# Optimization experiments

Measured on AMD Instinct MI355X. Metric: run time of the kernel, lower is better.

Reference implementation:

```python
import jax, jax.numpy as jnp
import numpy as np

B, HF, WF = 16, 32, 32
DIM, NH = 1024, 16
HD = DIM // NH  # 64


def axial_freqs(H, W, head_dim):
    # RotaryEmbedding(dim=head_dim//4, freqs_for='pixel', max_freq=H*W)
    d = head_dim // 4  # rotary dim per axis
    base = jnp.linspace(1.0, (H * W) / 2.0, d // 2) * jnp.pi  # [d//2]
    posH = jnp.linspace(-1.0, 1.0, H)
    posW = jnp.linspace(-1.0, 1.0, W)
    fH = jnp.repeat(posH[:, None] * base[None, :], 2, axis=-1)  # [H, d]
    fW = jnp.repeat(posW[:, None] * base[None, :], 2, axis=-1)  # [W, d]
    fH = jnp.broadcast_to(fH[:, None, :], (H, W, d))
    fW = jnp.broadcast_to(fW[None, :, :], (H, W, d))
    return jnp.concatenate([fH, fW], axis=-1)  # [H, W, 2d] = [H, W, head_dim//2]


def rotate_half(x):
    # interleaved pair rotation: (x1, x2) -> (-x2, x1)
    xr = x.reshape(*x.shape[:-1], -1, 2)
    x1, x2 = xr[..., 0], xr[..., 1]
    return jnp.stack([-x2, x1], axis=-1).reshape(x.shape)


def apply_rotary(freqs, t):
    # t: [B, h, H, W, hd]; freqs: [H, W, rot_dim]
    rd = freqs.shape[-1]
    t_rot, t_pass = t[..., :rd], t[..., rd:]
    t_rot = t_rot * jnp.cos(freqs) + rotate_half(t_rot) * jnp.sin(freqs)
    return jnp.concatenate([t_rot, t_pass], axis=-1)


def setup_inputs() -> dict:
    key = jax.random.key(0)
    k1, k2, k3 = jax.random.split(key, 3)
    s = 1.0 / np.sqrt(DIM)
    return {
        "x": jax.random.normal(k1, (B, HF * WF, DIM), jnp.float32),
        "w_qkv": jax.random.normal(k2, (3 * DIM, DIM), jnp.float32) * s,
        "w_proj": jax.random.normal(k3, (DIM, DIM), jnp.float32) * s,
        "b_proj": jnp.zeros((DIM,), jnp.float32),
    }


def reference(x, w_qkv, w_proj, b_proj):
    freqs = axial_freqs(HF, WF, HD)
    qkv = x @ w_qkv.T  # [B, N, 3*DIM]
    q, k, v = jnp.split(qkv, 3, axis=-1)

    def to_grid(t):  # [B, N, DIM] -> [B, h, H, W, hd]
        return t.reshape(B, HF, WF, NH, HD).transpose(0, 3, 1, 2, 4)

    q, k, v = to_grid(q), to_grid(k), to_grid(v)
    q = apply_rotary(freqs, q)
    k = apply_rotary(freqs, k)
    N = HF * WF
    q = q.reshape(B, NH, N, HD)
    k = k.reshape(B, NH, N, HD)
    v = v.reshape(B, NH, N, HD)

    scale = 1.0 / np.sqrt(HD)
    attn = jax.nn.softmax(jnp.einsum('bhnd,bhmd->bhnm', q, k) * scale, axis=-1)
    out = jnp.einsum('bhnm,bhmd->bhnd', attn, v)  # [B, h, N, hd]
    out = out.transpose(0, 2, 1, 3).reshape(B, N, DIM)
    return out @ w_proj.T + b_proj
```

## Files before the change

### kernel.cpp

```cpp
#include <hip/hip_runtime.h>
#include <hip/hip_bf16.h>
#include <math.h>

typedef __bf16 bf16;
typedef bf16 bf16x4 __attribute__((ext_vector_type(4)));
typedef bf16 bf16x8 __attribute__((ext_vector_type(8)));
typedef float f32x4 __attribute__((ext_vector_type(4)));

#define MFMA16(a, b, c) __builtin_amdgcn_mfma_f32_16x16x32_bf16((a), (b), (c), 0, 0, 0)

#define QSCALE 0.18033688011112042f

__device__ __forceinline__ void async16(const void* g, void* l) {
  __builtin_amdgcn_global_load_lds(
      (const __attribute__((address_space(1))) void*)g,
      (__attribute__((address_space(3))) void*)l, 16, 0, 0);
}

__global__ __launch_bounds__(256) void f2b_kernel(const float* __restrict__ in,
                                                  bf16* __restrict__ out, int n) {
  int i = (blockIdx.x * 256 + threadIdx.x) * 4;
  if (i >= n) return;
  f32x4 v = *(const f32x4*)(in + i);
  bf16x4 o = {(bf16)v[0], (bf16)v[1], (bf16)v[2], (bf16)v[3]};
  *(bf16x4*)(out + i) = o;
}

__global__ __launch_bounds__(256) void table_kernel(float* __restrict__ cosT,
                                                    float* __restrict__ sinT) {
  int idx = blockIdx.x * 256 + threadIdx.x;
  if (idx >= 1024 * 32) return;
  int n = idx >> 5, d = idx & 31;
  int hf = n >> 5, wf = n & 31;
  int bi = (d & 15) >> 1;
  float base = (1.0f + 73.0f * bi) * 3.14159265358979323846f;
  int p = (d < 16) ? hf : wf;
  float pos = (2.0f * (float)p - 31.0f) * (1.0f / 31.0f);
  float f = pos * base;
  cosT[idx] = cosf(f);
  sinT[idx] = sinf(f);
}

template <int EPI, int NBN>
__global__ __launch_bounds__(512, 2) void gemm_bt(
    const bf16* __restrict__ A, const bf16* __restrict__ W,
    bf16* __restrict__ oq, bf16* __restrict__ okk, bf16* __restrict__ ovt,
    const float* __restrict__ cosT, const float* __restrict__ sinT,
    float* __restrict__ outF, const float* __restrict__ bias) {
  constexpr int K = 1024;
  __shared__ bf16 As[4][256 * 32];
  __shared__ bf16 Bs[4][256 * 32];

  const int tid = threadIdx.x;
  const int lane = tid & 63;
  const int wid = tid >> 6;
  const int lo = lane & 15, hi = lane >> 4;
  const int wm = wid >> 2;
  const int wn = wid & 3;

  const int wg = blockIdx.x;
  const int xcd = wg & 7;
  const int i = wg >> 3;
  const int s = i >> 4;
  const int r = i & 15;
  const int bm = xcd * 8 + (s & 1) * 4 + (r & 3);
  const int bn = (s >> 1) * 4 + (r >> 2);

  const bf16* Ab = A + (size_t)bm * 256 * K;
  const bf16* Wb = W + (size_t)bn * 256 * K;

  const f32x4 fzero = {0.f, 0.f, 0.f, 0.f};
  f32x4 acc[8][4];
#pragma unroll
  for (int i2 = 0; i2 < 8; ++i2)
#pragma unroll
    for (int j = 0; j < 4; ++j) acc[i2][j] = fzero;

  size_t srcOff[2];
  int ldsOff[2];
#pragma unroll
  for (int i2 = 0; i2 < 2; ++i2) {
    const int c = i2 * 512 + tid;
    const int row = c >> 2, g = c & 3;
    const int gsrc = g ^ ((row >> 1) & 3);
    srcOff[i2] = (size_t)row * K + gsrc * 8;
    ldsOff[i2] = c * 8;
  }

  auto stageSlot = [&](int slot, int kh) {
#pragma unroll
    for (int i2 = 0; i2 < 2; ++i2)
      async16(Ab + srcOff[i2] + kh * 32, &As[slot][ldsOff[i2]]);
#pragma unroll
    for (int i2 = 0; i2 < 2; ++i2)
      async16(Wb + srcOff[i2] + kh * 32, &Bs[slot][ldsOff[i2]]);
  };

  auto compute = [&](int slot) {
    bf16x8 af[8], bf[4];
#pragma unroll
    for (int mf = 0; mf < 8; ++mf) {
      const int row = wm * 128 + mf * 16 + lo;
      const int g = hi ^ ((row >> 1) & 3);
      af[mf] = *(const bf16x8*)&As[slot][row * 32 + g * 8];
    }
#pragma unroll
    for (int nf = 0; nf < 4; ++nf) {
      const int row = wn * 64 + nf * 16 + lo;
      const int g = hi ^ ((row >> 1) & 3);
      bf[nf] = *(const bf16x8*)&Bs[slot][row * 32 + g * 8];
    }
    __builtin_amdgcn_s_setprio(1);
#pragma unroll
    for (int mf = 0; mf < 8; ++mf)
#pragma unroll
      for (int nf = 0; nf < 4; ++nf)
        acc[mf][nf] = MFMA16(af[mf], bf[nf], acc[mf][nf]);
    __builtin_amdgcn_s_setprio(0);
  };

  stageSlot(0, 0);
  stageSlot(1, 1);

  for (int kt = 0; kt < 7; ++kt) {
#pragma unroll
    for (int ph = 0; ph < 4; ++ph) {
      stageSlot((ph + 2) & 3, kt * 4 + ph + 2);
      asm volatile("s_waitcnt vmcnt(8)" ::: "memory");
      __builtin_amdgcn_s_barrier();
      compute(ph);
    }
  }
  stageSlot(2, 30);
  asm volatile("s_waitcnt vmcnt(8)" ::: "memory");
  __builtin_amdgcn_s_barrier();
  compute(0);
  stageSlot(3, 31);
  asm volatile("s_waitcnt vmcnt(8)" ::: "memory");
  __builtin_amdgcn_s_barrier();
  compute(1);
  asm volatile("s_waitcnt vmcnt(4)" ::: "memory");
  __builtin_amdgcn_s_barrier();
  compute(2);
  asm volatile("s_waitcnt vmcnt(0)" ::: "memory");
  __builtin_amdgcn_s_barrier();
  compute(3);

  const int rb0 = bm * 256 + wm * 128;
  const int jb0 = bn * 256 + wn * 64;

  if constexpr (EPI == 0) {
#pragma unroll
    for (int ac = 0; ac < 4; ++ac) {
      const int j = jb0 + ac * 16 + lo;
      const int which = j >> 10;
      const int f = j & 1023;
      const int h = f >> 6, d = f & 63;
#pragma unroll
      for (int ar = 0; ar < 8; ++ar) {
        const int rb = rb0 + ar * 16 + 4 * hi;
        f32x4 v = acc[ar][ac];
        if (which == 2) {
          const int b = rb >> 10, n0 = rb & 1023;
          bf16x4 pk = {(bf16)v[0], (bf16)v[1], (bf16)v[2], (bf16)v[3]};
          *(bf16x4*)(ovt + ((size_t)((b * 16 + h) * 64 + d)) * 1024 + n0) = pk;
        } else {
          bf16* dst = which ? okk : oq;
          const float sc = which ? 1.0f : QSCALE;
#pragma unroll
          for (int reg = 0; reg < 4; ++reg) {
            const int r2 = rb + reg;
            const int b = r2 >> 10, n = r2 & 1023;
            float val = v[reg];
            float res;
            if (d < 32) {
              float c = cosT[n * 32 + d];
              float sn = sinT[n * 32 + d];
              float pp = __shfl_xor(val, 1);
              res = (d & 1) ? fmaf(val, c, pp * sn) : fmaf(val, c, -(pp * sn));
            } else {
              res = val;
            }
            dst[((size_t)((b * 16 + h) * 1024 + n)) * 64 + d] = (bf16)(res * sc);
          }
        }
      }
    }
  } else {
#pragma unroll
    for (int ac = 0; ac < 4; ++ac) {
      const int j = jb0 + ac * 16 + lo;
      const float bv = bias[j];
#pragma unroll
      for (int ar = 0; ar < 8; ++ar) {
        const int rb = rb0 + ar * 16 + 4 * hi;
#pragma unroll
        for (int reg = 0; reg < 4; ++reg)
          outF[(size_t)(rb + reg) * 1024 + j] = acc[ar][ac][reg] + bv;
      }
    }
  }
}

__global__ __launch_bounds__(512, 4) void attn_fwd(const bf16* __restrict__ q,
                                                   const bf16* __restrict__ k,
                                                   const bf16* __restrict__ vt,
                                                   bf16* __restrict__ o) {
  __shared__ bf16 Kt[2][64 * 64];
  __shared__ bf16 Vt[2][64 * 64];
  __shared__ bf16 Pt[8][32 * 68];
  const int tid = threadIdx.x;
  const int lane = tid & 63, wid = tid >> 6;
  const int lo = lane & 15, hi = lane >> 4;
  const int j = blockIdx.x;
  const int bh = (j & 7) + ((j >> 5) << 3);
  const int qt = (j >> 3) & 3;
  const bf16* qg = q + (size_t)bh * 65536;
  const bf16* kg = k + (size_t)bh * 65536;
  const bf16* vg = vt + (size_t)bh * 65536;

  bf16x8 qf[2][2];
#pragma unroll
  for (int rg = 0; rg < 2; ++rg) {
    const int qrow = qt * 256 + wid * 32 + rg * 16 + lo;
#pragma unroll
    for (int ch = 0; ch < 2; ++ch)
      qf[rg][ch] = *(const bf16x8*)(qg + (size_t)qrow * 64 + ch * 32 + 8 * hi);
  }

  const int srow = tid >> 3;
  const int sgsrc = (tid & 7) ^ (srow & 7);
  auto stageKV = [&](int buf, int kv) {
    async16(kg + (size_t)(kv * 64 + srow) * 64 + sgsrc * 8, &Kt[buf][tid * 8]);
    async16(vg + (size_t)srow * 1024 + kv * 64 + sgsrc * 8, &Vt[buf][tid * 8]);
  };

  asm volatile("s_waitcnt vmcnt(0)" ::: "memory");
  stageKV(0, 0);

  const f32x4 fzero = {0.f, 0.f, 0.f, 0.f};
  f32x4 of[2][4];
  float psum[2][4];
#pragma unroll
  for (int rg = 0; rg < 2; ++rg)
#pragma unroll
    for (int r = 0; r < 4; ++r) {
      of[rg][r] = fzero;
      psum[rg][r] = 0.f;
    }

  const int m7 = lo & 7;

  for (int kv = 0; kv < 16; ++kv) {
    const int cur = kv & 1;
    if (kv < 15) {
      stageKV(cur ^ 1, kv + 1);
      asm volatile("s_waitcnt vmcnt(2)" ::: "memory");
    } else {
      asm volatile("s_waitcnt vmcnt(0)" ::: "memory");
    }
    __builtin_amdgcn_s_barrier();

#pragma unroll
    for (int kf = 0; kf < 4; ++kf) {
      const int r = kf * 16 + lo;
      bf16x8 kb0 = *(const bf16x8*)&Kt[cur][r * 64 + ((hi ^ m7) * 8)];
      bf16x8 kb1 = *(const bf16x8*)&Kt[cur][r * 64 + (((hi + 4) ^ m7) * 8)];
#pragma unroll
      for (int rg = 0; rg < 2; ++rg) {
        f32x4 z = fzero;
        z = MFMA16(qf[rg][0], kb0, z);
        z = MFMA16(qf[rg][1], kb1, z);
#pragma unroll
        for (int reg = 0; reg < 4; ++reg) {
          float p = __builtin_amdgcn_exp2f(z[reg]);
          psum[rg][reg] += p;
          Pt[wid][(rg * 16 + 4 * hi + reg) * 68 + kf * 16 + lo] = (bf16)p;
        }
      }
    }

    bf16x8 pa[2][2];
#pragma unroll
    for (int rg = 0; rg < 2; ++rg)
#pragma unroll
      for (int ch = 0; ch < 2; ++ch)
        pa[rg][ch] = *(const bf16x8*)&Pt[wid][(rg * 16 + lo) * 68 + ch * 32 + 8 * hi];
#pragma unroll
    for (int df = 0; df < 4; ++df) {
      const int r = df * 16 + lo;
      bf16x8 vb0 = *(const bf16x8*)&Vt[cur][r * 64 + ((hi ^ m7) * 8)];
      bf16x8 vb1 = *(const bf16x8*)&Vt[cur][r * 64 + (((hi + 4) ^ m7) * 8)];
#pragma unroll
      for (int rg = 0; rg < 2; ++rg) {
        of[rg][df] = MFMA16(pa[rg][0], vb0, of[rg][df]);
        of[rg][df] = MFMA16(pa[rg][1], vb1, of[rg][df]);
      }
    }
    __syncthreads();
  }

#pragma unroll
  for (int off = 1; off < 16; off <<= 1) {
#pragma unroll
    for (int rg = 0; rg < 2; ++rg)
#pragma unroll
      for (int reg = 0; reg < 4; ++reg) psum[rg][reg] += __shfl_xor(psum[rg][reg], off);
  }

  const int b = bh >> 4, h = bh & 15;
#pragma unroll
  for (int rg = 0; rg < 2; ++rg)
#pragma unroll
    for (int reg = 0; reg < 4; ++reg) {
      const int n = qt * 256 + wid * 32 + rg * 16 + 4 * hi + reg;
      const float inv = 1.0f / psum[rg][reg];
#pragma unroll
      for (int df = 0; df < 4; ++df)
        o[((size_t)(b * 1024 + n)) * 1024 + h * 64 + df * 16 + lo] =
            (bf16)(of[rg][df][reg] * inv);
    }
}

extern "C" void kernel_launch(void* const* d_in, const int* in_sizes, int n_in,
                              void* d_out, int out_size, void* d_ws, size_t ws_size,
                              hipStream_t stream) {
  (void)in_sizes; (void)n_in; (void)out_size; (void)ws_size;
  const float* x = (const float*)d_in[0];
  const float* wqkv = (const float*)d_in[1];
  const float* wproj = (const float*)d_in[2];
  const float* bproj = (const float*)d_in[3];

  char* ws = (char*)d_ws;
  bf16* xb = (bf16*)(ws);
  bf16* wqb = (bf16*)(ws + 33554432);
  bf16* wpb = (bf16*)(ws + 39845888);
  float* cosT = (float*)(ws + 41943040);
  float* sinT = (float*)(ws + 42074112);
  bf16* qb = (bf16*)(ws + 42205184);
  bf16* kb = (bf16*)(ws + 75759616);
  bf16* vtb = (bf16*)(ws + 109314048);

  f2b_kernel<<<16384, 256, 0, stream>>>(x, xb, 16 * 1024 * 1024);
  f2b_kernel<<<3072, 256, 0, stream>>>(wqkv, wqb, 3 * 1024 * 1024);
  f2b_kernel<<<1024, 256, 0, stream>>>(wproj, wpb, 1024 * 1024);
  table_kernel<<<128, 256, 0, stream>>>(cosT, sinT);

  gemm_bt<0, 12><<<768, 512, 0, stream>>>(xb, wqb, qb, kb, vtb, cosT, sinT,
                                          nullptr, nullptr);
  attn_fwd<<<1024, 512, 0, stream>>>(qb, kb, vtb, xb);
  gemm_bt<1, 4><<<256, 512, 0, stream>>>(xb, wpb, nullptr, nullptr, nullptr,
                                         nullptr, nullptr, (float*)d_out, bproj);
}
```

Measured before the change: 278.7 us.

## Restructure GEMM mainloop to double-buffered 64-wide K tiles with interleaved quarter-phase loads

Replaces the 4-slot, 32-wide K ring buffer with two 64-wide K buffers and a new swizzle based on row&7. Each K tile is split into four quarter phases: a quarter of the A fragments is read, the next tile's loads are issued in pieces between phases, and the wave synchronises with explicit lgkmcnt/vmcnt waits and barriers. The aim is to overlap LDS reads, global-to-LDS loads and MFMA work more finely and to halve the number of outer K iterations. The cost is many more barriers per tile, which could stall waves at 2 blocks per CU.

```diff
diff --git a/kernel.cpp b/kernel.cpp
--- a/kernel.cpp
+++ b/kernel.cpp
@@ -16,6 +16,11 @@
       (const __attribute__((address_space(1))) void*)g,
       (__attribute__((address_space(3))) void*)l, 16, 0, 0);
 }
+
+#define BAR __builtin_amdgcn_s_barrier()
+#define LGKM0 asm volatile("s_waitcnt lgkmcnt(0)" ::: "memory")
+#define LGKM8 asm volatile("s_waitcnt lgkmcnt(8)" ::: "memory")
+#define VMCNT(n) asm volatile("s_waitcnt vmcnt(" #n ")" ::: "memory")
 
 __global__ __launch_bounds__(256) void f2b_kernel(const float* __restrict__ in,
                                                   bf16* __restrict__ out, int n) {
@@ -48,8 +53,8 @@
     const float* __restrict__ cosT, const float* __restrict__ sinT,
     float* __restrict__ outF, const float* __restrict__ bias) {
   constexpr int K = 1024;
-  __shared__ bf16 As[4][256 * 32];
-  __shared__ bf16 Bs[4][256 * 32];
+  __shared__ bf16 As[2][256 * 64];
+  __shared__ bf16 Bs[2][256 * 64];
 
   const int tid = threadIdx.x;
   const int lane = tid & 63;
@@ -61,10 +66,10 @@
   const int wg = blockIdx.x;
   const int xcd = wg & 7;
   const int i = wg >> 3;
-  const int s = i >> 4;
-  const int r = i & 15;
-  const int bm = xcd * 8 + (s & 1) * 4 + (r & 3);
-  const int bn = (s >> 1) * 4 + (r >> 2);
+  const int s4 = i >> 4;
+  const int r4 = i & 15;
+  const int bm = xcd * 8 + (s4 & 1) * 4 + (r4 & 3);
+  const int bn = (s4 >> 1) * 4 + (r4 >> 2);
 
   const bf16* Ab = A + (size_t)bm * 256 * K;
   const bf16* Wb = W + (size_t)bn * 256 * K;
@@ -76,75 +81,89 @@
 #pragma unroll
     for (int j = 0; j < 4; ++j) acc[i2][j] = fzero;
 
-  size_t srcOff[2];
-  int ldsOff[2];
-#pragma unroll
-  for (int i2 = 0; i2 < 2; ++i2) {
-    const int c = i2 * 512 + tid;
-    const int row = c >> 2, g = c & 3;
-    const int gsrc = g ^ ((row >> 1) & 3);
-    srcOff[i2] = (size_t)row * K + gsrc * 8;
-    ldsOff[i2] = c * 8;
-  }
-
-  auto stageSlot = [&](int slot, int kh) {
-#pragma unroll
-    for (int i2 = 0; i2 < 2; ++i2)
-      async16(Ab + srcOff[i2] + kh * 32, &As[slot][ldsOff[i2]]);
-#pragma unroll
-    for (int i2 = 0; i2 < 2; ++i2)
-      async16(Wb + srcOff[i2] + kh * 32, &Bs[slot][ldsOff[i2]]);
-  };
-
-  auto compute = [&](int slot) {
-    bf16x8 af[8], bf[4];
-#pragma unroll
-    for (int mf = 0; mf < 8; ++mf) {
-      const int row = wm * 128 + mf * 16 + lo;
-      const int g = hi ^ ((row >> 1) & 3);
-      af[mf] = *(const bf16x8*)&As[slot][row * 32 + g * 8];
-    }
-#pragma unroll
-    for (int nf = 0; nf < 4; ++nf) {
-      const int row = wn * 64 + nf * 16 + lo;
-      const int g = hi ^ ((row >> 1) & 3);
-      bf[nf] = *(const bf16x8*)&Bs[slot][row * 32 + g * 8];
-    }
+  const int rr = (wid << 3) + ((lane >> 3) & 7);
+  const int sg = lane & 7;
+  auto stA = [&](int buf, int kt, int q23) {
+#pragma unroll
+    for (int i2 = 0; i2 < 2; ++i2) {
+      const int row = q23 * 64 + i2 * 128 + rr;
+      async16(Ab + (size_t)row * K + kt * 64 + (sg ^ (row & 7)) * 8,
+              &As[buf][row * 64 + sg * 8]);
+    }
+  };
+  auto stB = [&](int buf, int kt, int h) {
+#pragma unroll
+    for (int i2 = 0; i2 < 2; ++i2) {
+      const int row = h * 128 + i2 * 64 + rr;
+      async16(Wb + (size_t)row * K + kt * 64 + (sg ^ (row & 7)) * 8,
+              &Bs[buf][row * 64 + sg * 8]);
+    }
+  };
+
+  auto readA = [&](int buf, int mf, int s) -> bf16x8 {
+    const int row = wm * 128 + mf * 16 + lo;
+    const int g = (s * 4 + hi) ^ (lo & 7);
+    return *(const bf16x8*)&As[buf][row * 64 + g * 8];
+  };
+  auto readB = [&](int buf, int nf, int s) -> bf16x8 {
+    const int row = wn * 64 + nf * 16 + lo;
+    const int g = (s * 4 + hi) ^ (lo & 7);
+    return *(const bf16x8*)&Bs[buf][row * 64 + g * 8];
+  };
+
+  bf16x8 bfr[4][2];
+  bf16x8 a[2][2];
+  auto rdq = [&](int buf, int p) {
+#pragma unroll
+    for (int mi = 0; mi < 2; ++mi)
+#pragma unroll
+      for (int s = 0; s < 2; ++s) a[mi][s] = readA(buf, 2 * p + mi, s);
+  };
+  auto rdb = [&](int buf) {
+#pragma unroll
+    for (int nf = 0; nf < 4; ++nf)
+#pragma unroll
+      for (int s = 0; s < 2; ++s) bfr[nf][s] = readB(buf, nf, s);
+  };
+  auto mma = [&](int p) {
     __builtin_amdgcn_s_setprio(1);
 #pragma unroll
-    for (int mf = 0; mf < 8; ++mf)
+    for (int mi = 0; mi < 2; ++mi)
 #pragma unroll
       for (int nf = 0; nf < 4; ++nf)
-        acc[mf][nf] = MFMA16(af[mf], bf[nf], acc[mf][nf]);
+#pragma unroll
+        for (int s = 0; s < 2; ++s)
+          acc[2 * p + mi][nf] = MFMA16(a[mi][s], bfr[nf][s], acc[2 * p + mi][nf]);
     __builtin_amdgcn_s_setprio(0);
   };
 
-  stageSlot(0, 0);
-  stageSlot(1, 1);
-
-  for (int kt = 0; kt < 7; ++kt) {
-#pragma unroll
-    for (int ph = 0; ph < 4; ++ph) {
-      stageSlot((ph + 2) & 3, kt * 4 + ph + 2);
-      asm volatile("s_waitcnt vmcnt(8)" ::: "memory");
-      __builtin_amdgcn_s_barrier();
-      compute(ph);
-    }
-  }
-  stageSlot(2, 30);
-  asm volatile("s_waitcnt vmcnt(8)" ::: "memory");
-  __builtin_amdgcn_s_barrier();
-  compute(0);
-  stageSlot(3, 31);
-  asm volatile("s_waitcnt vmcnt(8)" ::: "memory");
-  __builtin_amdgcn_s_barrier();
-  compute(1);
-  asm volatile("s_waitcnt vmcnt(4)" ::: "memory");
-  __builtin_amdgcn_s_barrier();
-  compute(2);
-  asm volatile("s_waitcnt vmcnt(0)" ::: "memory");
-  __builtin_amdgcn_s_barrier();
-  compute(3);
+  stB(0, 0, 0); stB(0, 0, 1); stA(0, 0, 0); stA(0, 0, 1);
+  stB(1, 1, 0); stB(1, 1, 1); stA(1, 1, 0);
+  VMCNT(0);
+  BAR;
+
+  for (int t = 0; t < 7; ++t) {
+    const int c1 = 2 * t + 1, n0 = 2 * t + 2, n1 = 2 * t + 3;
+    rdq(0, 0); rdb(0); stA(1, c1, 1);
+    LGKM8; BAR; LGKM0; mma(0); BAR;
+    rdq(0, 1); stB(0, n0, 0); BAR; LGKM0; mma(1); BAR;
+    rdq(0, 2); stB(0, n0, 1); BAR; LGKM0; mma(2); BAR;
+    rdq(0, 3); stA(0, n0, 0); VMCNT(6); BAR; LGKM0; mma(3); BAR;
+    rdq(1, 0); rdb(1); stA(0, n0, 1);
+    LGKM8; BAR; LGKM0; mma(0); BAR;
+    rdq(1, 1); stB(1, n1, 0); BAR; LGKM0; mma(1); BAR;
+    rdq(1, 2); stB(1, n1, 1); BAR; LGKM0; mma(2); BAR;
+    rdq(1, 3); stA(1, n1, 0); VMCNT(6); BAR; LGKM0; mma(3); BAR;
+  }
+  rdq(0, 0); rdb(0); stA(1, 15, 1);
+  LGKM8; BAR; LGKM0; mma(0); BAR;
+  rdq(0, 1); BAR; LGKM0; mma(1); BAR;
+  rdq(0, 2); BAR; LGKM0; mma(2); BAR;
+  rdq(0, 3); VMCNT(0); BAR; LGKM0; mma(3); BAR;
+  rdq(1, 0); rdb(1); BAR; LGKM0; mma(0); BAR;
+  rdq(1, 1); BAR; LGKM0; mma(1); BAR;
+  rdq(1, 2); BAR; LGKM0; mma(2); BAR;
+  rdq(1, 3); LGKM0; mma(3);
 
   const int rb0 = bm * 256 + wm * 128;
   const int jb0 = bn * 256 + wn * 64;
```

After: 275.6 us. Within noise of the previous version (-1.1%).
